# Optimization experiments

Hardware: AMD Instinct MI355X
Metric: run time of the kernel (lower is better)

The kernel has to match this reference:

```python
import jax, jax.numpy as jnp
import numpy as np

KEHALF = 7.199822675975274  # half Coulomb constant, eV*Angstrom/e^2
SR_CUTOFF = 4.0
LR_CUTOFF = 10.0
N_ATOMS = 262144
N_PAIRS = 16777216


def setup_inputs() -> dict:
    key = jax.random.key(0)
    k1, k2, k3, k4 = jax.random.split(key, 4)
    # distances in (0.1, 12.1) Angstrom: spans both cutoffs, avoids r=0 singularity
    Dij = jax.random.uniform(k1, (N_PAIRS,), dtype=jnp.float32) * 12.0 + 0.1
    Qa = jax.random.normal(k2, (N_ATOMS,), dtype=jnp.float32) * 0.3  # partial charges
    idx_i = jax.random.randint(k3, (N_PAIRS,), 0, N_ATOMS, dtype=jnp.int64)
    idx_j = jax.random.randint(k4, (N_PAIRS,), 0, N_ATOMS, dtype=jnp.int64)
    return {"Dij": Dij, "Qa": Qa, "idx_i": idx_i, "idx_j": idx_j}


def _poly_cutoff(r, cutoff):
    x = r / cutoff
    return jnp.where(x < 1.0, 1.0 - x * x * x * (x * (6.0 * x - 15.0) + 10.0), 0.0)


def reference(Dij, Qa, idx_i, idx_j):
    lr2 = LR_CUTOFF * LR_CUTOFF
    Qi = Qa[idx_i]                      # [P]
    Qj = Qa[idx_j]                      # [P]
    Dij_sh = jnp.sqrt(Dij * Dij + 1.0)  # shielded distance
    switch = _poly_cutoff(Dij, SR_CUTOFF / 2.0)  # phi(2r) with cutoff sr
    cswitch = 1.0 - switch
    E_ord = 1.0 / Dij + Dij / lr2 - 2.0 / LR_CUTOFF
    E_sh = 1.0 / Dij_sh + Dij_sh / lr2 - 2.0 / LR_CUTOFF
    Eele = KEHALF * Qi * Qj * (switch * E_sh + cswitch * E_ord)
    Eele = jnp.where(Dij <= LR_CUTOFF, Eele, 0.0)
    # scatter-add per-pair energies to atoms
    return jax.ops.segment_sum(Eele, idx_i, num_segments=Qa.shape[0])
```

## Files before the change

kernel.cpp:

```cpp
#include <hip/hip_runtime.h>


#define KEHALF 7.199822675975274f
#define NB    128
#define BSH   11
#define BMASK 2047
#define CAP   126976
#define CURSTRIDE 16
#define SCH   2
#define SCAP  72
#define VSCALE 524288.0f
#define VINV   (1.0f / 524288.0f)
#define P1B   512
#define P1PAIRS 8192

__device__ __forceinline__ float radial(float d) {
    float dsh = sqrtf(d * d + 1.0f);
    float x   = 0.5f * d;
    float sw  = (x < 1.0f) ? 1.0f - x * x * x * (x * (6.0f * x - 15.0f) + 10.0f)
                           : 0.0f;
    float Eo = 1.0f / d   + d   * 0.01f - 0.2f;
    float Es = 1.0f / dsh + dsh * 0.01f - 0.2f;
    return sw * Es + (1.0f - sw) * Eo;
}

__global__ __launch_bounds__(P1B) void ee_bin(
    const float* __restrict__ Dij,
    const float* __restrict__ Qa,
    const int*   __restrict__ idx_i,
    const int*   __restrict__ idx_j,
    unsigned int* __restrict__ list,
    unsigned int* __restrict__ gcur,
    float*        __restrict__ out)
{
    __shared__ unsigned int stage[NB * SCAP];
    __shared__ int lcur[NB];
    __shared__ int gofs[NB];
    int tid = threadIdx.x;
    if (tid < NB) lcur[tid] = 0;
    __syncthreads();

    long blockBase = (long)blockIdx.x * P1PAIRS;

#pragma unroll
    for (int g = 0; g < 4; ++g) {
        long o = blockBase + ((long)(g * P1B + tid)) * 4;
        float4 d4 = *reinterpret_cast<const float4*>(Dij + o);
        int4   i4 = *reinterpret_cast<const int4*>(idx_i + o);
        int4   j4 = *reinterpret_cast<const int4*>(idx_j + o);
        float D[4]  = {d4.x, d4.y, d4.z, d4.w};
        int   II[4] = {i4.x, i4.y, i4.z, i4.w};
        int   JJ[4] = {j4.x, j4.y, j4.z, j4.w};
#pragma unroll
        for (int k = 0; k < 4; ++k) {
            float d = D[k];
            if (d <= 10.0f) {
                float w = Qa[JJ[k]] * radial(d);
                int v = __float2int_rn(w * VSCALE);
                int b  = II[k] >> BSH;
                int li = II[k] & BMASK;
                int slot = atomicAdd(&lcur[b], 1);
                if (slot < SCAP) {
                    stage[b * SCAP + slot] =
                        ((unsigned int)li << 21) | ((unsigned int)v & 0x1FFFFFu);
                } else {
                    atomicAdd(out + II[k], KEHALF * Qa[II[k]] * w);
                }
            }
        }
    }
    __syncthreads();

    if (tid < NB) {
        int n = lcur[tid];
        if (n > SCAP) n = SCAP;
        lcur[tid] = n;
        int padded = (n + 15) & ~15;
        gofs[tid] = (int)atomicAdd(&gcur[tid * CURSTRIDE], (unsigned int)padded);
    }
    __syncthreads();

    int wave = tid >> 6, lane = tid & 63;
    for (int b = wave; b < NB; b += (P1B / 64)) {
        int n = lcur[b];
        int padded = (n + 15) & ~15;
        int go = gofs[b];
        long rb = (long)b * CAP;
        for (int i = lane; i < padded; i += 64) {
            unsigned int val = (i < n) ? stage[b * SCAP + i] : 0u;
            int pos = go + i;
            if (pos < CAP)
                list[rb + pos] = val;
        }
    }
}

__global__ __launch_bounds__(512) void ee_acc(
    const unsigned int* __restrict__ list,
    const unsigned int* __restrict__ gcur,
    int* __restrict__ partials)
{
    __shared__ int acc[1 << BSH];
    int b = blockIdx.x / SCH;
    int s = blockIdx.x % SCH;
    int t = threadIdx.x;
#pragma unroll
    for (int r = 0; r < (1 << BSH) / 512; ++r) acc[t + r * 512] = 0;
    __syncthreads();

    int n = (int)gcur[b * CURSTRIDE];
    if (n > CAP) n = CAP;
    int nq = n >> 2;
    int per = (nq + SCH - 1) / SCH;
    int q0 = s * per;
    int q1 = q0 + per; if (q1 > nq) q1 = nq;

    const uint4* lp4 = reinterpret_cast<const uint4*>(list + (long)b * CAP);
    for (int q = q0 + t; q < q1; q += 512) {
        uint4 u4 = lp4[q];
        unsigned int us[4] = {u4.x, u4.y, u4.z, u4.w};
#pragma unroll
        for (int k = 0; k < 4; ++k) {
            unsigned int u = us[k];
            int li = (int)(u >> 21);
            int v  = ((int)(u << 11)) >> 11;
            atomicAdd(&acc[li], v);
        }
    }
    __syncthreads();

    int* pp = partials + ((long)b * SCH + s) * (1 << BSH);
#pragma unroll
    for (int r = 0; r < (1 << BSH) / 512; ++r) pp[t + r * 512] = acc[t + r * 512];
}

__global__ __launch_bounds__(256) void ee_final(
    const int* __restrict__ partials,
    const float* __restrict__ Qa,
    float* __restrict__ out, int nAtoms)
{
    int q = blockIdx.x * blockDim.x + threadIdx.x;
    int n4 = nAtoms >> 2;
    if (q >= n4) return;
    int a0 = q << 2;
    int b  = a0 >> BSH;
    int li = a0 & BMASK;
    long base = (long)(b * SCH) * (1 << BSH) + li;
    int4 s = {0, 0, 0, 0};
#pragma unroll
    for (int r = 0; r < SCH; ++r) {
        int4 p = *reinterpret_cast<const int4*>(partials + base + (long)r * (1 << BSH));
        s.x += p.x; s.y += p.y; s.z += p.z; s.w += p.w;
    }
    float4 qv = reinterpret_cast<const float4*>(Qa)[q];
    float4 sp = reinterpret_cast<const float4*>(out)[q];
    float4 o;
    o.x = KEHALF * qv.x * ((float)s.x * VINV) + sp.x;
    o.y = KEHALF * qv.y * ((float)s.y * VINV) + sp.y;
    o.z = KEHALF * qv.z * ((float)s.z * VINV) + sp.z;
    o.w = KEHALF * qv.w * ((float)s.w * VINV) + sp.w;
    reinterpret_cast<float4*>(out)[q] = o;
}

#define FP_SCALE 4194304.0f
#define FP_INV   (1.0f / 4194304.0f)

__global__ __launch_bounds__(256) void ee_pair_fix(
    const float* __restrict__ Dij,
    const float* __restrict__ Qa,
    const int*   __restrict__ idx_i,
    const int*   __restrict__ idx_j,
    int*         __restrict__ acc,
    int P)
{
    long base = ((long)blockIdx.x * blockDim.x + threadIdx.x) * 4;
    if (base >= P) return;
    float4 d4 = *reinterpret_cast<const float4*>(Dij + base);
    int4   i4 = *reinterpret_cast<const int4*>(idx_i + base);
    int4   j4 = *reinterpret_cast<const int4*>(idx_j + base);
    float D[4]  = {d4.x, d4.y, d4.z, d4.w};
    int   ii[4] = {i4.x, i4.y, i4.z, i4.w};
    int   jj[4] = {j4.x, j4.y, j4.z, j4.w};
#pragma unroll
    for (int k = 0; k < 4; ++k) {
        float d = D[k];
        if (d > 10.0f) continue;
        float e = KEHALF * Qa[ii[k]] * Qa[jj[k]] * radial(d);
        atomicAdd(acc + ii[k], __float2int_rn(e * FP_SCALE));
    }
}

__global__ __launch_bounds__(256) void ee_convert(
    const int* __restrict__ acc, float* __restrict__ out, int nAtoms)
{
    int n4 = nAtoms >> 2;
    int q = blockIdx.x * blockDim.x + threadIdx.x;
    if (q >= n4) return;
    int4 a = reinterpret_cast<const int4*>(acc)[q];
    float4 o;
    o.x = (float)a.x * FP_INV;
    o.y = (float)a.y * FP_INV;
    o.z = (float)a.z * FP_INV;
    o.w = (float)a.w * FP_INV;
    reinterpret_cast<float4*>(out)[q] = o;
}

__global__ __launch_bounds__(256) void ee_pair_direct(
    const float* __restrict__ Dij,
    const float* __restrict__ Qa,
    const int*   __restrict__ idx_i,
    const int*   __restrict__ idx_j,
    float*       __restrict__ out,
    int P)
{
    long t = (long)blockIdx.x * blockDim.x + threadIdx.x;
    if (t >= P) return;
    float d = Dij[t];
    if (d > 10.0f) return;
    atomicAdd(out + idx_i[t], KEHALF * Qa[idx_i[t]] * Qa[idx_j[t]] * radial(d));
}

extern "C" void kernel_launch(void* const* d_in, const int* in_sizes, int n_in,
                              void* d_out, int out_size, void* d_ws, size_t ws_size,
                              hipStream_t stream) {
    const float* Dij   = (const float*)d_in[0];
    const float* Qa    = (const float*)d_in[1];
    const int*   idx_i = (const int*)d_in[2];
    const int*   idx_j = (const int*)d_in[3];
    float*       out   = (float*)d_out;

    int P      = in_sizes[0];
    int nAtoms = in_sizes[1];

    size_t listBytes = (size_t)NB * CAP * sizeof(unsigned int);
    size_t partBytes = (size_t)NB * SCH * (1 << BSH) * sizeof(int);
    size_t curBytes  = (size_t)NB * CURSTRIDE * sizeof(unsigned int);

    if (ws_size >= listBytes + partBytes + curBytes &&
        nAtoms == NB * (1 << BSH) && (P % P1PAIRS) == 0) {
        unsigned int* list = (unsigned int*)d_ws;
        int*          part = (int*)((char*)d_ws + listBytes);
        unsigned int* gcur = (unsigned int*)((char*)d_ws + listBytes + partBytes);
        hipMemsetAsync(gcur, 0, curBytes, stream);
        hipMemsetAsync(out, 0, (size_t)out_size * sizeof(float), stream);
        int grid1 = P / P1PAIRS;
        ee_bin<<<grid1, P1B, 0, stream>>>(Dij, Qa, idx_i, idx_j, list, gcur, out);
        ee_acc<<<NB * SCH, 512, 0, stream>>>(list, gcur, part);
        ee_final<<<(nAtoms / 4 + 255) / 256, 256, 0, stream>>>(part, Qa, out, nAtoms);
    } else if (ws_size >= (size_t)nAtoms * sizeof(int) &&
               (nAtoms & 3) == 0 && (P & 3) == 0) {
        int* acc = (int*)d_ws;
        hipMemsetAsync(acc, 0, (size_t)nAtoms * sizeof(int), stream);
        int grid = (P / 4 + 255) / 256;
        ee_pair_fix<<<grid, 256, 0, stream>>>(Dij, Qa, idx_i, idx_j, acc, P);
        ee_convert<<<(nAtoms / 4 + 255) / 256, 256, 0, stream>>>(acc, out, nAtoms);
    } else {
        hipMemsetAsync(out, 0, (size_t)out_size * sizeof(float), stream);
        int grid = (P + 255) / 256;
        ee_pair_direct<<<grid, 256, 0, stream>>>(Dij, Qa, idx_i, idx_j, out, P);
    }
}
```

Baseline: 290.4 us.

## Batch gathers ahead of compute and use fast rcp/rsq intrinsics in bin kernel

In the binning kernel, all 16 pair loads per thread, including the Qa[idx_j] gathers, are now issued up front before any compute. This raises memory-level parallelism for the random gathers. The radial function uses hardware reciprocal and reciprocal-sqrt approximations and rewrites the shielded term algebraically so it needs no sqrt or divide. A launch-bounds occupancy hint is added. The approximate intrinsics may slightly change precision, and the extra live registers may reduce occupancy.

Measured after the change: 281.4 us. 3.1% less time.

```diff
diff --git a/kernel.cpp b/kernel.cpp
--- a/kernel.cpp
+++ b/kernel.cpp
@@ -14,17 +14,18 @@
 #define P1B   512
 #define P1PAIRS 8192
 
-__device__ __forceinline__ float radial(float d) {
-    float dsh = sqrtf(d * d + 1.0f);
-    float x   = 0.5f * d;
-    float sw  = (x < 1.0f) ? 1.0f - x * x * x * (x * (6.0f * x - 15.0f) + 10.0f)
-                           : 0.0f;
-    float Eo = 1.0f / d   + d   * 0.01f - 0.2f;
-    float Es = 1.0f / dsh + dsh * 0.01f - 0.2f;
+__device__ __forceinline__ float radial_fast(float d) {
+    float d2p1 = d * d + 1.0f;
+    float rsq  = __builtin_amdgcn_rsqf(d2p1);
+    float x    = 0.5f * d;
+    float sw   = (x < 1.0f) ? 1.0f - x * x * x * (x * (6.0f * x - 15.0f) + 10.0f)
+                            : 0.0f;
+    float Eo = __builtin_amdgcn_rcpf(d) + d * 0.01f - 0.2f;
+    float Es = rsq * (1.0f + 0.01f * d2p1) - 0.2f;
     return sw * Es + (1.0f - sw) * Eo;
 }
 
-__global__ __launch_bounds__(P1B) void ee_bin(
+__global__ __launch_bounds__(P1B, 4) void ee_bin(
     const float* __restrict__ Dij,
     const float* __restrict__ Qa,
     const int*   __restrict__ idx_i,
@@ -42,30 +43,40 @@
 
     long blockBase = (long)blockIdx.x * P1PAIRS;
 
+    float D[16];
+    int   II[16];
+    float QJ[16];
+
 #pragma unroll
     for (int g = 0; g < 4; ++g) {
         long o = blockBase + ((long)(g * P1B + tid)) * 4;
+        int4 j4 = *reinterpret_cast<const int4*>(idx_j + o);
+        QJ[g * 4 + 0] = Qa[j4.x];
+        QJ[g * 4 + 1] = Qa[j4.y];
+        QJ[g * 4 + 2] = Qa[j4.z];
+        QJ[g * 4 + 3] = Qa[j4.w];
         float4 d4 = *reinterpret_cast<const float4*>(Dij + o);
         int4   i4 = *reinterpret_cast<const int4*>(idx_i + o);
-        int4   j4 = *reinterpret_cast<const int4*>(idx_j + o);
-        float D[4]  = {d4.x, d4.y, d4.z, d4.w};
-        int   II[4] = {i4.x, i4.y, i4.z, i4.w};
-        int   JJ[4] = {j4.x, j4.y, j4.z, j4.w};
-#pragma unroll
-        for (int k = 0; k < 4; ++k) {
-            float d = D[k];
-            if (d <= 10.0f) {
-                float w = Qa[JJ[k]] * radial(d);
-                int v = __float2int_rn(w * VSCALE);
-                int b  = II[k] >> BSH;
-                int li = II[k] & BMASK;
-                int slot = atomicAdd(&lcur[b], 1);
-                if (slot < SCAP) {
-                    stage[b * SCAP + slot] =
-                        ((unsigned int)li << 21) | ((unsigned int)v & 0x1FFFFFu);
-                } else {
-                    atomicAdd(out + II[k], KEHALF * Qa[II[k]] * w);
-                }
+        D[g * 4 + 0] = d4.x; D[g * 4 + 1] = d4.y;
+        D[g * 4 + 2] = d4.z; D[g * 4 + 3] = d4.w;
+        II[g * 4 + 0] = i4.x; II[g * 4 + 1] = i4.y;
+        II[g * 4 + 2] = i4.z; II[g * 4 + 3] = i4.w;
+    }
+
+#pragma unroll
+    for (int m = 0; m < 16; ++m) {
+        float d = D[m];
+        if (d <= 10.0f) {
+            float w = QJ[m] * radial_fast(d);
+            int v = __float2int_rn(w * VSCALE);
+            int b  = II[m] >> BSH;
+            int li = II[m] & BMASK;
+            int slot = atomicAdd(&lcur[b], 1);
+            if (slot < SCAP) {
+                stage[b * SCAP + slot] =
+                    ((unsigned int)li << 21) | ((unsigned int)v & 0x1FFFFFu);
+            } else {
+                atomicAdd(out + II[m], KEHALF * Qa[II[m]] * w);
             }
         }
     }
@@ -165,6 +176,16 @@
 #define FP_SCALE 4194304.0f
 #define FP_INV   (1.0f / 4194304.0f)
 
+__device__ __forceinline__ float radial_exact(float d) {
+    float dsh = sqrtf(d * d + 1.0f);
+    float x   = 0.5f * d;
+    float sw  = (x < 1.0f) ? 1.0f - x * x * x * (x * (6.0f * x - 15.0f) + 10.0f)
+                           : 0.0f;
+    float Eo = 1.0f / d   + d   * 0.01f - 0.2f;
+    float Es = 1.0f / dsh + dsh * 0.01f - 0.2f;
+    return sw * Es + (1.0f - sw) * Eo;
+}
+
 __global__ __launch_bounds__(256) void ee_pair_fix(
     const float* __restrict__ Dij,
     const float* __restrict__ Qa,
@@ -185,7 +206,7 @@
     for (int k = 0; k < 4; ++k) {
         float d = D[k];
         if (d > 10.0f) continue;
-        float e = KEHALF * Qa[ii[k]] * Qa[jj[k]] * radial(d);
+        float e = KEHALF * Qa[ii[k]] * Qa[jj[k]] * radial_exact(d);
         atomicAdd(acc + ii[k], __float2int_rn(e * FP_SCALE));
     }
 }
@@ -217,7 +238,7 @@
     if (t >= P) return;
     float d = Dij[t];
     if (d > 10.0f) return;
-    atomicAdd(out + idx_i[t], KEHALF * Qa[idx_i[t]] * Qa[idx_j[t]] * radial(d));
+    atomicAdd(out + idx_i[t], KEHALF * Qa[idx_i[t]] * Qa[idx_j[t]] * radial_exact(d));
 }
 
 extern "C" void kernel_launch(void* const* d_in, const int* in_sizes, int n_in,
```
